# Kernel tuning notes

Hardware: AMD Instinct MI355X
Metric: run time of the kernel (lower is better)

The kernel has to match this reference:

```python
import jax, jax.numpy as jnp
import numpy as np

N_EMBD = 384
NUM_HEADS = 6


def setup_inputs() -> dict:
    key = jax.random.key(0)
    k1, k2, k3 = jax.random.split(key, 3)
    b, t = 128, 256
    X = jax.random.normal(k1, (b, t, N_EMBD), dtype=jnp.float32)
    Wqkv = jax.random.normal(k2, (N_EMBD, 3 * N_EMBD), dtype=jnp.float32) * 0.02
    Wproj = jax.random.normal(k3, (N_EMBD, N_EMBD), dtype=jnp.float32) * 0.02
    return {"X": X, "Wqkv": Wqkv, "Wproj": Wproj}


def reference(X, Wqkv, Wproj):
    b, t, c = X.shape
    d = c // NUM_HEADS
    # fused QKV projection; split order in the source is K, Q, V
    qkv = X @ Wqkv  # (b, t, 3c)
    K, Q, V = jnp.split(qkv, 3, axis=-1)
    # (b, t, H, d) -> (b, H, t, d)
    K = K.reshape(b, t, NUM_HEADS, d).transpose(0, 2, 1, 3)
    Q = Q.reshape(b, t, NUM_HEADS, d).transpose(0, 2, 1, 3)
    V = V.reshape(b, t, NUM_HEADS, d).transpose(0, 2, 1, 3)
    # NOTE: faithful quirk — scale by full embed dim c, not head_size
    scale = c ** (-0.5)
    W = jnp.einsum("bhqd,bhkd->bhqk", Q, K) * scale  # (b, H, t, t)
    causal = jnp.tril(jnp.ones((t, t), dtype=bool))
    W = jnp.where(causal, W, -jnp.inf)
    W = jax.nn.softmax(W, axis=-1)
    # dropout layers are identity in eval mode
    OUT = jnp.einsum("bhqk,bhkd->bhqd", W, V)  # (b, H, t, d)
    OUT = OUT.transpose(0, 2, 1, 3).reshape(b, t, c)
    return OUT @ Wproj
```

## Files before the change

### kernel.cpp

```cpp
#include <hip/hip_runtime.h>
#include <hip/hip_bf16.h>

#define BATCH 128
#define TSEQ  256
#define NEMBD 384
#define NHEAD 6
#define HDIM  64
#define C3    1152
#define MROWS 32768
#define KGTOT 48
#define NBH   768
#define BHSZ  16384

#define NA_CH  (MROWS * KGTOT)
#define NW1_CH (C3 * KGTOT)
#define NW2_CH (NEMBD * KGTOT)

#define XBLOCKS 2048
#define WBLOCKS 288

typedef __attribute__((ext_vector_type(8))) short short8v;
typedef __attribute__((ext_vector_type(4))) float float4v;


__device__ __forceinline__ unsigned short f2bf(float f) {
  __hip_bfloat16 h = __float2bfloat16(f);
  unsigned short u;
  __builtin_memcpy(&u, &h, 2);
  return u;
}

__device__ __forceinline__ void convB_body(const float* __restrict__ W,
                                           unsigned short* __restrict__ out,
                                           int N, int idx) {
  const int nl  = idx & 127;
  const int kgg = (idx >> 7) % KGTOT;
  const int nb  = idx / (128 * KGTOT);
  const int n = nb * 128 + nl;
  short8v v;
#pragma unroll
  for (int j = 0; j < 8; ++j)
    v[j] = (short)f2bf(W[(size_t)(kgg * 8 + j) * N + n]);
  *reinterpret_cast<short8v*>(out + (size_t)idx * 8) = v;
}

__global__ __launch_bounds__(256)
void convert_all(const float* __restrict__ X, const float* __restrict__ W1,
                 const float* __restrict__ W2, unsigned short* __restrict__ Abf,
                 unsigned short* __restrict__ W1T, unsigned short* __restrict__ W2T) {
  const int tid = threadIdx.x;
  if (blockIdx.x < XBLOCKS) {
    __shared__ __attribute__((aligned(16))) unsigned short T[16][392];
    const int rb = blockIdx.x;
    const float* Xb = X + (size_t)rb * 16 * NEMBD;
#pragma unroll
    for (int i = 0; i < 6; ++i) {
      const int f4 = i * 256 + tid;
      const float4 v = reinterpret_cast<const float4*>(Xb)[f4];
      const int r = f4 / 96;
      const int c = (f4 % 96) * 4;
      ushort4 u;
      u.x = f2bf(v.x); u.y = f2bf(v.y); u.z = f2bf(v.z); u.w = f2bf(v.w);
      *reinterpret_cast<ushort4*>(&T[r][c]) = u;
    }
    __syncthreads();
#pragma unroll
    for (int i = 0; i < 3; ++i) {
      const int c2   = i * 256 + tid;
      const int kgg  = c2 >> 4;
      const int ml16 = c2 & 15;
      const short8v v = *reinterpret_cast<const short8v*>(&T[ml16][kgg * 8]);
      const int m  = rb * 16 + ml16;
      const int mb = m >> 7;
      const int ml = m & 127;
      *reinterpret_cast<short8v*>(Abf + ((size_t)(mb * KGTOT + kgg) * 128 + ml) * 8) = v;
    }
  } else {
    const int wi = (blockIdx.x - XBLOCKS) * 256 + tid;
    if (wi < NW1_CH) convB_body(W1, W1T, C3, wi);
    else             convB_body(W2, W2T, NEMBD, wi - NW1_CH);
  }
}


#define GEMM_STAGE(Ab, Bb, kb, ASL, BSL)                                               \
  _Pragma("unroll") for (int r = 0; r < 2; ++r) {                                      \
    const int i = r * 256 + tid;                                                       \
    const size_t goff = ((size_t)((kb) * 4 + (i >> 7)) * 128 + (i & 127)) * 8;         \
    __builtin_amdgcn_global_load_lds(                                                  \
        (const __attribute__((address_space(1))) unsigned int*)((Ab) + goff),          \
        (__attribute__((address_space(3))) unsigned int*)((ASL) + i * 8), 16, 0, 0);   \
    __builtin_amdgcn_global_load_lds(                                                  \
        (const __attribute__((address_space(1))) unsigned int*)((Bb) + goff),          \
        (__attribute__((address_space(3))) unsigned int*)((BSL) + i * 8), 16, 0, 0);   \
  }

#define GEMM_CORE(Ab, Bb)                                                              \
  __shared__ __attribute__((aligned(16))) unsigned short S[16384];                     \
  const int tid  = threadIdx.x;                                                        \
  const int wave = tid >> 6;                                                           \
  const int lane = tid & 63;                                                           \
  const int wm  = (wave & 1) * 64;                                                     \
  const int wn  = (wave >> 1) * 64;                                                    \
  const int l15 = lane & 15;                                                           \
  const int lq  = lane >> 4;                                                           \
  float4v acc[4][4];                                                                   \
  _Pragma("unroll") for (int i = 0; i < 4; ++i)                                        \
    _Pragma("unroll") for (int j = 0; j < 4; ++j)                                      \
      acc[i][j] = (float4v){0.f, 0.f, 0.f, 0.f};                                       \
  GEMM_STAGE(Ab, Bb, 0, S, S + 4096)                                                   \
  for (int kb = 0; kb < KGTOT / 4; ++kb) {                                             \
    const int cur = (kb & 1) * 8192;                                                   \
    const int nxt = 8192 - cur;                                                        \
    __syncthreads();                                                                   \
    if (kb + 1 < KGTOT / 4) {                                                          \
      GEMM_STAGE(Ab, Bb, kb + 1, S + nxt, S + nxt + 4096)                              \
    }                                                                                  \
    short8v af[4], bfr[4];                                                             \
    _Pragma("unroll") for (int mi = 0; mi < 4; ++mi)                                   \
      af[mi] = *reinterpret_cast<const short8v*>(                                      \
          S + cur + (size_t)(lq * 128 + wm + mi * 16 + l15) * 8);                      \
    _Pragma("unroll") for (int ni = 0; ni < 4; ++ni)                                   \
      bfr[ni] = *reinterpret_cast<const short8v*>(                                     \
          S + cur + 4096 + (size_t)(lq * 128 + wn + ni * 16 + l15) * 8);               \
    _Pragma("unroll") for (int mi = 0; mi < 4; ++mi)                                   \
      _Pragma("unroll") for (int ni = 0; ni < 4; ++ni)                                 \
        acc[mi][ni] = __builtin_amdgcn_mfma_f32_16x16x32_bf16(af[mi], bfr[ni],         \
                                                              acc[mi][ni], 0, 0, 0);   \
  }

__global__ __launch_bounds__(256)
void gemm_qkv(const unsigned short* __restrict__ A,
              const unsigned short* __restrict__ B,
              unsigned short* __restrict__ KQV) {
  const int ord   = blockIdx.x;
  const int xcd   = ord & 7;
  const int g     = ord >> 3;
  const int mtile = xcd * 32 + (g & 31);
  const int ntile = g >> 5;
  const unsigned short* Ab = A + (size_t)mtile * (KGTOT * 128 * 8);
  const unsigned short* Bb = B + (size_t)ntile * (KGTOT * 128 * 8);
  GEMM_CORE(Ab, Bb)
  if (ntile >= 6) {
    unsigned short* Vb = KQV + (size_t)(2 * NBH) * BHSZ;
    const int hh0 = (ntile - 6) * 2;
    const int bb  = mtile >> 1;
    const int tg0 = (mtile & 1) * 16;
    __syncthreads();
#pragma unroll
    for (int ni = 0; ni < 4; ++ni) {
      const int lc = wn + ni * 16 + l15;
      const int hh = lc >> 6;
      const int d  = lc & 63;
#pragma unroll
      for (int mi = 0; mi < 4; ++mi) {
        const int ttl = wm + mi * 16 + lq * 4;
        const int tg  = ttl >> 3;
        const int tl0 = ttl & 7;
        ushort4 u;
        u.x = f2bf(acc[mi][ni][0]); u.y = f2bf(acc[mi][ni][1]);
        u.z = f2bf(acc[mi][ni][2]); u.w = f2bf(acc[mi][ni][3]);
        *reinterpret_cast<ushort4*>(
            S + (size_t)(((hh * 16 + tg) * 64 + d) * 8 + tl0)) = u;
      }
    }
    __syncthreads();
#pragma unroll
    for (int it = 0; it < 8; ++it) {
      const int f  = it * 2048 + tid * 8;
      const int cc = f >> 3;
      const int d  = cc & 63;
      const int tg = (cc >> 6) & 15;
      const int hh = cc >> 10;
      *reinterpret_cast<short8v*>(
          Vb + (size_t)(bb * NHEAD + hh0 + hh) * BHSZ + (tg0 + tg) * 512 + d * 8) =
          *reinterpret_cast<const short8v*>(S + f);
    }
  } else {
    const int type = (ntile >= 3) ? 1 : 0;
    const float sc = type ? 0.051031036307982884f : 1.0f;
    unsigned short* outb = KQV + (size_t)type * NBH * BHSZ;
    const int hp = ntile - type * 3;
    const int bb = mtile >> 1;
    const int t0 = (mtile & 1) * 128;
    __syncthreads();
#pragma unroll
    for (int ni = 0; ni < 4; ++ni) {
      const int lc = wn + ni * 16 + l15;
      const int c8 = lc >> 3;
      const int dl = lc & 7;
#pragma unroll
      for (int mi = 0; mi < 4; ++mi) {
        const int lr0 = wm + lq * 4 + mi * 16;
#pragma unroll
        for (int r = 0; r < 4; ++r) {
          const int c  = c8 * 128 + lr0 + r;
          const int cs = c ^ (((c >> 7) ^ (c >> 3)) & 7);
          S[(size_t)cs * 8 + dl] = f2bf(acc[mi][ni][r] * sc);
        }
      }
    }
    __syncthreads();
#pragma unroll
    for (int it = 0; it < 8; ++it) {
      const int f   = it * 2048 + tid * 8;
      const int cc  = f >> 3;
      const int cs  = cc ^ (((cc >> 7) ^ (cc >> 3)) & 7);
      const int c8  = cc >> 7;
      const int lr  = cc & 127;
      const int hh  = hp * 2 + (c8 >> 3);
      const int dg  = c8 & 7;
      *reinterpret_cast<short8v*>(
          outb + (size_t)(bb * NHEAD + hh) * BHSZ + dg * 2048 + (size_t)(t0 + lr) * 8) =
          *reinterpret_cast<const short8v*>(S + (size_t)cs * 8);
    }
  }
}

__global__ __launch_bounds__(256)
void gemm_proj(const unsigned short* __restrict__ A,
               const unsigned short* __restrict__ B,
               float* __restrict__ C, int N) {
  const int ord   = blockIdx.x;
  const int xcd   = ord & 7;
  const int g     = ord >> 3;
  const int mtile = xcd * 32 + (g & 31);
  const int ntile = g >> 5;
  const unsigned short* Ab = A + (size_t)mtile * (KGTOT * 128 * 8);
  const unsigned short* Bb = B + (size_t)ntile * (KGTOT * 128 * 8);
  GEMM_CORE(Ab, Bb)
  float* Sf = reinterpret_cast<float*>(S);
#pragma unroll
  for (int pass = 0; pass < 2; ++pass) {
    __syncthreads();
    if ((wave & 1) == pass) {
#pragma unroll
      for (int mi = 0; mi < 4; ++mi)
#pragma unroll
        for (int ni = 0; ni < 4; ++ni)
#pragma unroll
          for (int r = 0; r < 4; ++r)
            Sf[(lq * 4 + mi * 16 + r) * 128 + (wn + ni * 16 + l15)] = acc[mi][ni][r];
    }
    __syncthreads();
    const int rowstart = mtile * 128 + pass * 64;
#pragma unroll
    for (int it = 0; it < 8; ++it) {
      const int f  = it * 1024 + tid * 4;
      const int lr = f >> 7;
      const int lc = f & 127;
      *reinterpret_cast<float4*>(&C[(size_t)(rowstart + lr) * N + ntile * 128 + lc]) =
          *reinterpret_cast<const float4*>(&Sf[f]);
    }
  }
}

__global__ __launch_bounds__(256, 3)
void attn_mfma(const unsigned short* __restrict__ KQV,
               unsigned short* __restrict__ Obf) {
  const int bh   = blockIdx.x;
  const int b    = bh / NHEAD;
  const int h    = bh - b * NHEAD;
  const int tid  = threadIdx.x;
  const int wave = tid >> 6;
  const int lane = tid & 63;
  const int l15  = lane & 15;
  const int lq   = lane >> 4;

  __shared__ __attribute__((aligned(16))) unsigned short Kls[16384];
  __shared__ __attribute__((aligned(16))) unsigned short Pt[4][1024];

  const unsigned short* Kb = KQV + (size_t)bh * BHSZ;
  const unsigned short* Qb = KQV + (size_t)(NBH + bh) * BHSZ;
  const unsigned short* Vb = KQV + (size_t)(2 * NBH + bh) * BHSZ;

#pragma unroll
  for (int r = 0; r < 8; ++r) {
    const int i = r * 256 + tid;
    __builtin_amdgcn_global_load_lds(
        (const __attribute__((address_space(1))) unsigned int*)(Kb + (size_t)i * 8),
        (__attribute__((address_space(3))) unsigned int*)(Kls + i * 8), 16, 0, 0);
  }
  __syncthreads();

  unsigned short* Pw = Pt[wave];

  for (int j = 0; j < 4; ++j) {
    short8v qa[2];
#pragma unroll
    for (int s = 0; s < 2; ++s)
      qa[s] = *reinterpret_cast<const short8v*>(
          Qb + (size_t)(s * 4 + lq) * 2048 + (size_t)(j * 64 + wave * 16 + l15) * 8);

    float4v o[4];
#pragma unroll
    for (int nf = 0; nf < 4; ++nf) o[nf] = (float4v){0.f, 0.f, 0.f, 0.f};
    float4v lp = (float4v){0.f, 0.f, 0.f, 0.f};

    for (int kt = 0; kt <= j; ++kt) {
      short8v vf[2][4];
#pragma unroll
      for (int s = 0; s < 2; ++s)
#pragma unroll
        for (int nf = 0; nf < 4; ++nf)
          vf[s][nf] = *reinterpret_cast<const short8v*>(
              Vb + (size_t)(kt * 8 + s * 4 + lq) * 512 + (size_t)(nf * 16 + l15) * 8);

      float4v sf[4];
#pragma unroll
      for (int nf = 0; nf < 4; ++nf) sf[nf] = (float4v){0.f, 0.f, 0.f, 0.f};
#pragma unroll
      for (int s = 0; s < 2; ++s) {
        short8v kf[4];
#pragma unroll
        for (int nf = 0; nf < 4; ++nf)
          kf[nf] = *reinterpret_cast<const short8v*>(
              Kls + (size_t)(s * 4 + lq) * 2048 + (size_t)(kt * 64 + nf * 16 + l15) * 8);
#pragma unroll
        for (int nf = 0; nf < 4; ++nf)
          sf[nf] = __builtin_amdgcn_mfma_f32_16x16x32_bf16(qa[s], kf[nf], sf[nf], 0, 0, 0);
      }

      if (kt == j) {
        const int qit = wave * 16 + lq * 4;
#pragma unroll
        for (int nf = 0; nf < 4; ++nf) {
          const int key = nf * 16 + l15;
#pragma unroll
          for (int r = 0; r < 4; ++r)
            if (key > qit + r) sf[nf][r] = -INFINITY;
        }
      }

#pragma unroll
      for (int nf = 0; nf < 4; ++nf) {
        const int kg  = nf * 2 + (l15 >> 3);
        const int pos = l15 & 7;
#pragma unroll
        for (int r = 0; r < 4; ++r) {
          const float p = __expf(sf[nf][r]);
          lp[r] += p;
          Pw[(kg * 16 + lq * 4 + r) * 8 + pos] = f2bf(p);
        }
      }

#pragma unroll
      for (int s = 0; s < 2; ++s) {
        short8v pa = *reinterpret_cast<const short8v*>(
            Pw + (size_t)((s * 4 + lq) * 16 + l15) * 8);
#pragma unroll
        for (int nf = 0; nf < 4; ++nf)
          o[nf] = __builtin_amdgcn_mfma_f32_16x16x32_bf16(pa, vf[s][nf], o[nf], 0, 0, 0);
      }
    }

#pragma unroll
    for (int off = 1; off <= 8; off <<= 1)
#pragma unroll
      for (int r = 0; r < 4; ++r)
        lp[r] += __shfl_xor(lp[r], off);
    float4v inv;
#pragma unroll
    for (int r = 0; r < 4; ++r) inv[r] = 1.f / lp[r];

#pragma unroll
    for (int nf = 0; nf < 4; ++nf) {
      const int d   = nf * 16 + l15;
      const int ggl = d >> 3;
      const int pos = d & 7;
#pragma unroll
      for (int r = 0; r < 4; ++r) {
        const int chunk = (ggl * 16 + lq * 4 + r) ^ ggl;
        Pw[chunk * 8 + pos] = f2bf(o[nf][r] * inv[r]);
      }
    }
    const int mb  = b * 2 + (j >> 1);
    const int ml0 = (j & 1) * 64 + wave * 16;
#pragma unroll
    for (int t = 0; t < 2; ++t) {
      const int cc  = t * 64 + lane;
      const int ggl = cc >> 4;
      const int mll = cc & 15;
      *reinterpret_cast<short8v*>(
          Obf + ((size_t)(mb * KGTOT) + h * 8 + ggl) * 1024 + (size_t)(ml0 + mll) * 8) =
          *reinterpret_cast<const short8v*>(Pw + (size_t)(cc ^ ggl) * 8);
    }
  }
}


extern "C" void kernel_launch(void* const* d_in, const int* in_sizes, int n_in,
                              void* d_out, int out_size, void* d_ws, size_t ws_size,
                              hipStream_t stream) {
  const float* X     = (const float*)d_in[0];
  const float* Wqkv  = (const float*)d_in[1];
  const float* Wproj = (const float*)d_in[2];
  float* out = (float*)d_out;

  unsigned short* KQV    = (unsigned short*)d_ws;
  unsigned short* Abf    = (unsigned short*)((char*)d_ws + 75497472);
  unsigned short* WqkvT  = (unsigned short*)((char*)d_ws + 75497472 + 25165824);
  unsigned short* WprojT = (unsigned short*)((char*)d_ws + 75497472 + 25165824 + 884736);
  unsigned short* Obf    = Abf;

  dim3 blk(256);
  convert_all<<<dim3(XBLOCKS + WBLOCKS), blk, 0, stream>>>(
      X, Wqkv, Wproj, Abf, WqkvT, WprojT);
  gemm_qkv<<<dim3(2304), blk, 0, stream>>>(Abf, WqkvT, KQV);
  attn_mfma<<<dim3(NBH), blk, 0, stream>>>(KQV, Obf);
  gemm_proj<<<dim3(768), blk, 0, stream>>>(Obf, WprojT, out, NEMBD);
}
```

Measured before the change: 173.6 us.

## Enlarge GEMM tiles to 256x128 with 512-thread blocks for QKV and proj

Both GEMMs now use 256-row by 128-column output tiles computed by 8 waves in 512-thread blocks, where they previously used 128x128 tiles with 4 waves. The B tile is now loaded once per 256 rows, which halves B traffic and global-to-LDS staging per output element. The epilogues are restructured into two or four passes through shared memory so each pass writes a full batch-head slab. The block-to-XCD mapping is redone for the new grid sizes. In exchange, LDS use per block rises and the grid shrinks, which may reduce occupancy and load balance.

Measured after the change: 179.6 us. 1.03x slower.

```diff
diff --git a/kernel.cpp b/kernel.cpp
--- a/kernel.cpp
+++ b/kernel.cpp
@@ -83,157 +83,166 @@
 }
 
 
-#define GEMM_STAGE(Ab, Bb, kb, ASL, BSL)                                               \
-  _Pragma("unroll") for (int r = 0; r < 2; ++r) {                                      \
-    const int i = r * 256 + tid;                                                       \
-    const size_t goff = ((size_t)((kb) * 4 + (i >> 7)) * 128 + (i & 127)) * 8;         \
+#define GEMM_STAGE256(Ab2, Bb, kb, AL, BL)                                             \
+  _Pragma("unroll") for (int p = 0; p < 2; ++p) {                                      \
+    const int i   = p * 512 + tid;                                                     \
+    const int kg  = i >> 8;                                                            \
+    const int row = i & 255;                                                           \
+    const size_t goff = ((size_t)((row >> 7) * KGTOT + (kb) * 4 + kg) * 128            \
+                        + (row & 127)) * 8;                                            \
     __builtin_amdgcn_global_load_lds(                                                  \
-        (const __attribute__((address_space(1))) unsigned int*)((Ab) + goff),          \
-        (__attribute__((address_space(3))) unsigned int*)((ASL) + i * 8), 16, 0, 0);   \
+        (const __attribute__((address_space(1))) unsigned int*)((Ab2) + goff),         \
+        (__attribute__((address_space(3))) unsigned int*)((AL) + (kg * 256 + row) * 8),\
+        16, 0, 0);                                                                     \
+  }                                                                                    \
+  {                                                                                    \
+    const int kgB  = tid >> 7;                                                         \
+    const int rowB = tid & 127;                                                        \
+    const size_t goffB = ((size_t)((kb) * 4 + kgB) * 128 + rowB) * 8;                  \
     __builtin_amdgcn_global_load_lds(                                                  \
-        (const __attribute__((address_space(1))) unsigned int*)((Bb) + goff),          \
-        (__attribute__((address_space(3))) unsigned int*)((BSL) + i * 8), 16, 0, 0);   \
-  }
-
-#define GEMM_CORE(Ab, Bb)                                                              \
-  __shared__ __attribute__((aligned(16))) unsigned short S[16384];                     \
+        (const __attribute__((address_space(1))) unsigned int*)((Bb) + goffB),         \
+        (__attribute__((address_space(3))) unsigned int*)((BL) + (kgB * 128 + rowB) * 8),\
+        16, 0, 0);                                                                     \
+  }
+
+#define GEMM_CORE256(Ab2, Bb)                                                          \
+  __shared__ __attribute__((aligned(16))) unsigned short S[24576];                     \
   const int tid  = threadIdx.x;                                                        \
   const int wave = tid >> 6;                                                           \
   const int lane = tid & 63;                                                           \
-  const int wm  = (wave & 1) * 64;                                                     \
-  const int wn  = (wave >> 1) * 64;                                                    \
+  const int wm  = (wave & 3) * 64;                                                     \
+  const int wn  = (wave >> 2) * 64;                                                    \
   const int l15 = lane & 15;                                                           \
   const int lq  = lane >> 4;                                                           \
   float4v acc[4][4];                                                                   \
   _Pragma("unroll") for (int i = 0; i < 4; ++i)                                        \
     _Pragma("unroll") for (int j = 0; j < 4; ++j)                                      \
       acc[i][j] = (float4v){0.f, 0.f, 0.f, 0.f};                                       \
-  GEMM_STAGE(Ab, Bb, 0, S, S + 4096)                                                   \
+  GEMM_STAGE256(Ab2, Bb, 0, S, S + 8192)                                               \
   for (int kb = 0; kb < KGTOT / 4; ++kb) {                                             \
-    const int cur = (kb & 1) * 8192;                                                   \
-    const int nxt = 8192 - cur;                                                        \
+    const int cur = (kb & 1) * 12288;                                                  \
+    const int nxt = 12288 - cur;                                                       \
     __syncthreads();                                                                   \
     if (kb + 1 < KGTOT / 4) {                                                          \
-      GEMM_STAGE(Ab, Bb, kb + 1, S + nxt, S + nxt + 4096)                              \
+      GEMM_STAGE256(Ab2, Bb, kb + 1, S + nxt, S + nxt + 8192)                          \
     }                                                                                  \
     short8v af[4], bfr[4];                                                             \
     _Pragma("unroll") for (int mi = 0; mi < 4; ++mi)                                   \
       af[mi] = *reinterpret_cast<const short8v*>(                                      \
-          S + cur + (size_t)(lq * 128 + wm + mi * 16 + l15) * 8);                      \
+          S + cur + (size_t)(lq * 256 + wm + mi * 16 + l15) * 8);                      \
     _Pragma("unroll") for (int ni = 0; ni < 4; ++ni)                                   \
       bfr[ni] = *reinterpret_cast<const short8v*>(                                     \
-          S + cur + 4096 + (size_t)(lq * 128 + wn + ni * 16 + l15) * 8);               \
+          S + cur + 8192 + (size_t)(lq * 128 + wn + ni * 16 + l15) * 8);               \
     _Pragma("unroll") for (int mi = 0; mi < 4; ++mi)                                   \
       _Pragma("unroll") for (int ni = 0; ni < 4; ++ni)                                 \
         acc[mi][ni] = __builtin_amdgcn_mfma_f32_16x16x32_bf16(af[mi], bfr[ni],         \
                                                               acc[mi][ni], 0, 0, 0);   \
   }
 
-__global__ __launch_bounds__(256)
+__global__ __launch_bounds__(512)
 void gemm_qkv(const unsigned short* __restrict__ A,
               const unsigned short* __restrict__ B,
               unsigned short* __restrict__ KQV) {
   const int ord   = blockIdx.x;
   const int xcd   = ord & 7;
   const int g     = ord >> 3;
-  const int mtile = xcd * 32 + (g & 31);
-  const int ntile = g >> 5;
-  const unsigned short* Ab = A + (size_t)mtile * (KGTOT * 128 * 8);
-  const unsigned short* Bb = B + (size_t)ntile * (KGTOT * 128 * 8);
-  GEMM_CORE(Ab, Bb)
+  const int m2    = xcd * 16 + g / 9;
+  const int ntile = g % 9;
+  const unsigned short* Ab2 = A + (size_t)(m2 * 2) * (KGTOT * 128 * 8);
+  const unsigned short* Bb  = B + (size_t)ntile * (KGTOT * 128 * 8);
+  GEMM_CORE256(Ab2, Bb)
+  const int half = wave >> 2;
   if (ntile >= 6) {
     unsigned short* Vb = KQV + (size_t)(2 * NBH) * BHSZ;
     const int hh0 = (ntile - 6) * 2;
-    const int bb  = mtile >> 1;
-    const int tg0 = (mtile & 1) * 16;
     __syncthreads();
 #pragma unroll
-    for (int ni = 0; ni < 4; ++ni) {
-      const int lc = wn + ni * 16 + l15;
-      const int hh = lc >> 6;
-      const int d  = lc & 63;
-#pragma unroll
-      for (int mi = 0; mi < 4; ++mi) {
-        const int ttl = wm + mi * 16 + lq * 4;
-        const int tg  = ttl >> 3;
-        const int tl0 = ttl & 7;
-        ushort4 u;
-        u.x = f2bf(acc[mi][ni][0]); u.y = f2bf(acc[mi][ni][1]);
-        u.z = f2bf(acc[mi][ni][2]); u.w = f2bf(acc[mi][ni][3]);
-        *reinterpret_cast<ushort4*>(
-            S + (size_t)(((hh * 16 + tg) * 64 + d) * 8 + tl0)) = u;
-      }
-    }
-    __syncthreads();
-#pragma unroll
-    for (int it = 0; it < 8; ++it) {
-      const int f  = it * 2048 + tid * 8;
-      const int cc = f >> 3;
-      const int d  = cc & 63;
-      const int tg = (cc >> 6) & 15;
-      const int hh = cc >> 10;
-      *reinterpret_cast<short8v*>(
-          Vb + (size_t)(bb * NHEAD + hh0 + hh) * BHSZ + (tg0 + tg) * 512 + d * 8) =
-          *reinterpret_cast<const short8v*>(S + f);
+    for (int p = 0; p < 2; ++p) {
+      if (half == p) {
+#pragma unroll
+        for (int ni = 0; ni < 4; ++ni) {
+          const int d = ni * 16 + l15;
+#pragma unroll
+          for (int mi = 0; mi < 4; ++mi) {
+            const int ttl = wm + mi * 16 + lq * 4;
+            const int tg  = ttl >> 3;
+            const int tl0 = ttl & 7;
+            ushort4 u;
+            u.x = f2bf(acc[mi][ni][0]); u.y = f2bf(acc[mi][ni][1]);
+            u.z = f2bf(acc[mi][ni][2]); u.w = f2bf(acc[mi][ni][3]);
+            *reinterpret_cast<ushort4*>(S + (size_t)((tg * 64 + d) * 8 + tl0)) = u;
+          }
+        }
+      }
+      __syncthreads();
+      const size_t base = (size_t)(m2 * NHEAD + hh0 + p) * BHSZ;
+#pragma unroll
+      for (int it = 0; it < 4; ++it) {
+        const int f = it * 512 + tid;
+        *reinterpret_cast<short8v*>(Vb + base + (size_t)f * 8) =
+            *reinterpret_cast<const short8v*>(S + (size_t)f * 8);
+      }
+      __syncthreads();
     }
   } else {
     const int type = (ntile >= 3) ? 1 : 0;
     const float sc = type ? 0.051031036307982884f : 1.0f;
     unsigned short* outb = KQV + (size_t)type * NBH * BHSZ;
     const int hp = ntile - type * 3;
-    const int bb = mtile >> 1;
-    const int t0 = (mtile & 1) * 128;
     __syncthreads();
 #pragma unroll
-    for (int ni = 0; ni < 4; ++ni) {
-      const int lc = wn + ni * 16 + l15;
-      const int c8 = lc >> 3;
-      const int dl = lc & 7;
-#pragma unroll
-      for (int mi = 0; mi < 4; ++mi) {
-        const int lr0 = wm + lq * 4 + mi * 16;
-#pragma unroll
-        for (int r = 0; r < 4; ++r) {
-          const int c  = c8 * 128 + lr0 + r;
-          const int cs = c ^ (((c >> 7) ^ (c >> 3)) & 7);
-          S[(size_t)cs * 8 + dl] = f2bf(acc[mi][ni][r] * sc);
+    for (int p = 0; p < 2; ++p) {
+      if (half == p) {
+#pragma unroll
+        for (int ni = 0; ni < 4; ++ni) {
+          const int d  = ni * 16 + l15;
+          const int c8 = d >> 3;
+          const int dl = d & 7;
+#pragma unroll
+          for (int mi = 0; mi < 4; ++mi) {
+            const int lr0 = wm + mi * 16 + lq * 4;
+#pragma unroll
+            for (int r = 0; r < 4; ++r) {
+              const int c  = c8 * 256 + lr0 + r;
+              const int cs = c ^ (((c >> 8) ^ (c >> 3)) & 7);
+              S[(size_t)cs * 8 + dl] = f2bf(acc[mi][ni][r] * sc);
+            }
+          }
         }
       }
-    }
-    __syncthreads();
-#pragma unroll
-    for (int it = 0; it < 8; ++it) {
-      const int f   = it * 2048 + tid * 8;
-      const int cc  = f >> 3;
-      const int cs  = cc ^ (((cc >> 7) ^ (cc >> 3)) & 7);
-      const int c8  = cc >> 7;
-      const int lr  = cc & 127;
-      const int hh  = hp * 2 + (c8 >> 3);
-      const int dg  = c8 & 7;
-      *reinterpret_cast<short8v*>(
-          outb + (size_t)(bb * NHEAD + hh) * BHSZ + dg * 2048 + (size_t)(t0 + lr) * 8) =
-          *reinterpret_cast<const short8v*>(S + (size_t)cs * 8);
-    }
-  }
-}
-
-__global__ __launch_bounds__(256)
+      __syncthreads();
+      const size_t base = (size_t)(m2 * NHEAD + hp * 2 + p) * BHSZ;
+#pragma unroll
+      for (int it = 0; it < 4; ++it) {
+        const int cc = it * 512 + tid;
+        const int cs = cc ^ (((cc >> 8) ^ (cc >> 3)) & 7);
+        const int c8 = cc >> 8;
+        const int lr = cc & 255;
+        *reinterpret_cast<short8v*>(outb + base + c8 * 2048 + (size_t)lr * 8) =
+            *reinterpret_cast<const short8v*>(S + (size_t)cs * 8);
+      }
+      __syncthreads();
+    }
+  }
+}
+
+__global__ __launch_bounds__(512)
 void gemm_proj(const unsigned short* __restrict__ A,
                const unsigned short* __restrict__ B,
                float* __restrict__ C, int N) {
   const int ord   = blockIdx.x;
   const int xcd   = ord & 7;
   const int g     = ord >> 3;
-  const int mtile = xcd * 32 + (g & 31);
-  const int ntile = g >> 5;
-  const unsigned short* Ab = A + (size_t)mtile * (KGTOT * 128 * 8);
-  const unsigned short* Bb = B + (size_t)ntile * (KGTOT * 128 * 8);
-  GEMM_CORE(Ab, Bb)
+  const int m2    = xcd * 16 + g / 3;
+  const int ntile = g % 3;
+  const unsigned short* Ab2 = A + (size_t)(m2 * 2) * (KGTOT * 128 * 8);
+  const unsigned short* Bb  = B + (size_t)ntile * (KGTOT * 128 * 8);
+  GEMM_CORE256(Ab2, Bb)
   float* Sf = reinterpret_cast<float*>(S);
 #pragma unroll
-  for (int pass = 0; pass < 2; ++pass) {
+  for (int p = 0; p < 4; ++p) {
     __syncthreads();
-    if ((wave & 1) == pass) {
+    if ((wave & 3) == p) {
 #pragma unroll
       for (int mi = 0; mi < 4; ++mi)
 #pragma unroll
@@ -243,14 +252,14 @@
             Sf[(lq * 4 + mi * 16 + r) * 128 + (wn + ni * 16 + l15)] = acc[mi][ni][r];
     }
     __syncthreads();
-    const int rowstart = mtile * 128 + pass * 64;
-#pragma unroll
-    for (int it = 0; it < 8; ++it) {
-      const int f  = it * 1024 + tid * 4;
-      const int lr = f >> 7;
-      const int lc = f & 127;
+    const int rowstart = m2 * 256 + p * 64;
+#pragma unroll
+    for (int it = 0; it < 4; ++it) {
+      const int f  = it * 512 + tid;
+      const int lr = f >> 5;
+      const int lc = (f & 31) * 4;
       *reinterpret_cast<float4*>(&C[(size_t)(rowstart + lr) * N + ntile * 128 + lc]) =
-          *reinterpret_cast<const float4*>(&Sf[f]);
+          *reinterpret_cast<const float4*>(&Sf[f * 4]);
     }
   }
 }
@@ -403,10 +412,9 @@
   unsigned short* WprojT = (unsigned short*)((char*)d_ws + 75497472 + 25165824 + 884736);
   unsigned short* Obf    = Abf;
 
-  dim3 blk(256);
-  convert_all<<<dim3(XBLOCKS + WBLOCKS), blk, 0, stream>>>(
+  convert_all<<<dim3(XBLOCKS + WBLOCKS), dim3(256), 0, stream>>>(
       X, Wqkv, Wproj, Abf, WqkvT, WprojT);
-  gemm_qkv<<<dim3(2304), blk, 0, stream>>>(Abf, WqkvT, KQV);
-  attn_mfma<<<dim3(NBH), blk, 0, stream>>>(KQV, Obf);
-  gemm_proj<<<dim3(768), blk, 0, stream>>>(Obf, WprojT, out, NEMBD);
-}
+  gemm_qkv<<<dim3(1152), dim3(512), 0, stream>>>(Abf, WqkvT, KQV);
+  attn_mfma<<<dim3(NBH), dim3(256), 0, stream>>>(KQV, Obf);
+  gemm_proj<<<dim3(384), dim3(512), 0, stream>>>(Obf, WprojT, out, NEMBD);
+}
```
